# Performance work log

Hardware: AMD Instinct MI355X
Metric: run time of the kernel (lower is better)

## Reference

```python
import jax, jax.numpy as jnp
import numpy as np

N_NODES = 50000
N_EDGES = 800000

def _sage_conv(x, src, dst, W, b, n_nodes):
    # DGL SAGEConv aggregator_type='gcn':
    #   h_neigh = (sum_{u in N(v)} x_u + x_v) / (in_deg(v) + 1)
    #   out = h_neigh @ W.T + b   (fc_self unused for gcn aggregator)
    agg = jax.ops.segment_sum(x[src], dst, num_segments=n_nodes)  # [N, d]
    deg = jax.ops.segment_sum(jnp.ones((src.shape[0],), x.dtype), dst, num_segments=n_nodes)
    h = (agg + x) / (deg + 1.0)[:, None]
    return h @ W.T + b

def setup_inputs() -> dict:
    key = jax.random.key(0)
    ks = jax.random.split(key, 9)
    d_in, d_hid, d_out = 128, 128, 64
    x = jax.random.normal(ks[0], (N_NODES, d_in), dtype=jnp.float32)
    src = jax.random.randint(ks[1], (N_EDGES,), 0, N_NODES, dtype=jnp.int32)
    dst = jax.random.randint(ks[2], (N_EDGES,), 0, N_NODES, dtype=jnp.int32)
    def glorot(k, shape):
        fan = shape[0] + shape[1]
        return jax.random.normal(k, shape, dtype=jnp.float32) * jnp.sqrt(2.0 / fan)
    W1 = glorot(ks[3], (d_hid, d_in))
    b1 = jnp.zeros((d_hid,), jnp.float32)
    W2 = glorot(ks[4], (d_hid, d_hid))
    b2 = jnp.zeros((d_hid,), jnp.float32)
    W3 = glorot(ks[5], (d_out, d_hid))
    b3 = jnp.zeros((d_out,), jnp.float32)
    return {"x": x, "src": src, "dst": dst, "W1": W1, "b1": b1,
            "W2": W2, "b2": b2, "W3": W3, "b3": b3}

def reference(x, src, dst, W1, b1, W2, b2, W3, b3):
    n = x.shape[0]
    h = jax.nn.relu(_sage_conv(x, src, dst, W1, b1, n))
    h = jax.nn.relu(_sage_conv(h, src, dst, W2, b2, n))
    h = jax.nn.sigmoid(_sage_conv(h, src, dst, W3, b3, n))
    return h
```

## Files before the change

kernel.cpp:

```cpp
#include <hip/hip_runtime.h>
#include <hip/hip_bf16.h>
#include <math.h>


#define NFEAT 128
#define BSH   7
#define NBUKP 512
#define EPB2  1024
#define CAP   4000

typedef __attribute__((ext_vector_type(8))) short bf16x8;
typedef __attribute__((ext_vector_type(4))) float f32x4;

__device__ __forceinline__ unsigned short f2bf(float f) {
    unsigned u = __float_as_uint(f);
    u += 0x7fffu + ((u >> 16) & 1u);
    return (unsigned short)(u >> 16);
}
__device__ __forceinline__ float bflo(unsigned u) { return __uint_as_float(u << 16); }
__device__ __forceinline__ float bfhi(unsigned u) { return __uint_as_float(u & 0xffff0000u); }


__global__ __launch_bounds__(256) void build_scatter(const int* __restrict__ src,
                                                     const int* __restrict__ dst,
                                                     int* __restrict__ cursor,
                                                     unsigned long long* __restrict__ pairs,
                                                     int E) {
    __shared__ int hist[NBUKP];
    __shared__ int sc[NBUKP];
    __shared__ int lcur[NBUKP];
    __shared__ int lbase[NBUKP];
    __shared__ unsigned long long stage[EPB2];
    __shared__ int destIdx[EPB2];
    __shared__ int nLocalSh;

    const int t = threadIdx.x;
    hist[t] = 0; hist[t + 256] = 0;
    lcur[t] = 0; lcur[t + 256] = 0;
    __syncthreads();

    const int base = blockIdx.x * EPB2;
    int bb[EPB2 / 256];
    unsigned long long pr[EPB2 / 256];
#pragma unroll
    for (int j = 0; j < EPB2 / 256; ++j) {
        int e = base + t + 256 * j;
        bb[j] = -1;
        if (e < E) {
            int s = src[e], d = dst[e];
            int b = d >> BSH;
            bb[j] = b;
            pr[j] = ((unsigned long long)(unsigned)d << 32) | (unsigned)s;
            atomicAdd(&hist[b], 1);
        }
    }
    __syncthreads();
    sc[t] = hist[t]; sc[t + 256] = hist[t + 256];
    __syncthreads();
    for (int off = 1; off < NBUKP; off <<= 1) {
        int v0 = (t >= off) ? sc[t - off] : 0;
        int v1 = (t + 256 >= off) ? sc[t + 256 - off] : 0;
        __syncthreads();
        sc[t] += v0; sc[t + 256] += v1;
        __syncthreads();
    }
    if (t == 255) nLocalSh = sc[NBUKP - 1];
    sc[t] -= hist[t]; sc[t + 256] -= hist[t + 256];
    for (int b = t; b < NBUKP; b += 256) {
        int h = hist[b];
        if (h > 0) lbase[b] = atomicAdd(&cursor[b], h);
    }
    __syncthreads();
#pragma unroll
    for (int j = 0; j < EPB2 / 256; ++j) {
        int b = bb[j];
        if (b >= 0) {
            int slot = atomicAdd(&lcur[b], 1);
            int spos = sc[b] + slot;
            stage[spos] = pr[j];
            int rel = lbase[b] + slot;
            destIdx[spos] = (rel < CAP) ? (b * CAP + rel) : -1;
        }
    }
    __syncthreads();
    const int nLocal = nLocalSh;
#pragma unroll
    for (int j = 0; j < EPB2 / 256; ++j) {
        int i = t + 256 * j;
        if (i < nLocal && destIdx[i] >= 0) pairs[destIdx[i]] = stage[i];
    }
}


__global__ __launch_bounds__(256) void build_csr(const unsigned long long* __restrict__ pairs,
                                                 const int* __restrict__ cursor,
                                                 int* __restrict__ row_beg,
                                                 int* __restrict__ row_end,
                                                 float* __restrict__ deg_inv,
                                                 int* __restrict__ col_idx, int N) {
    __shared__ unsigned long long pairsL[CAP];
    __shared__ int srcS[CAP];
    __shared__ int nhist[128];
    __shared__ int npref[128];
    __shared__ int ncur[128];

    const int t = threadIdx.x;
    const int b = blockIdx.x;
    const int nodeBase = b << BSH;
    const int eBeg = b * CAP;
    int eCnt = cursor[b];
    if (eCnt > CAP) eCnt = CAP;

    if (t < 128) { nhist[t] = 0; ncur[t] = 0; }
    __syncthreads();

    for (int i = t; i < eCnt; i += 256) {
        unsigned long long p = pairs[eBeg + i];
        pairsL[i] = p;
        atomicAdd(&nhist[(int)(p >> 32) - nodeBase], 1);
    }
    __syncthreads();
    if (t < 128) npref[t] = nhist[t];
    __syncthreads();
    for (int off = 1; off < 128; off <<= 1) {
        int v = (t < 128 && t >= off) ? npref[t - off] : 0;
        __syncthreads();
        if (t < 128) npref[t] += v;
        __syncthreads();
    }
    if (t < 128) npref[t] -= nhist[t];
    if (t < 128 && nodeBase + t < N) {
        row_beg[nodeBase + t] = eBeg + npref[t];
        row_end[nodeBase + t] = eBeg + npref[t] + nhist[t];
        deg_inv[nodeBase + t] = 1.0f / (float)(nhist[t] + 1);
    }
    __syncthreads();
    for (int i = t; i < eCnt; i += 256) {
        unsigned long long p = pairsL[i];
        int d = (int)(p >> 32) - nodeBase;
        int slot = atomicAdd(&ncur[d], 1);
        srcS[npref[d] + slot] = (int)(unsigned)p;
    }
    __syncthreads();
    for (int i = t; i < eCnt; i += 256) col_idx[eBeg + i] = srcS[i];
}


__global__ __launch_bounds__(256) void cvt_all_kernel(const float* __restrict__ x,
                                                      const float* __restrict__ W1,
                                                      const float* __restrict__ W2,
                                                      const float* __restrict__ W3,
                                                      ushort* __restrict__ xb,
                                                      ushort* __restrict__ w1,
                                                      ushort* __restrict__ w2,
                                                      ushort* __restrict__ w3,
                                                      int nx, int n1, int n2, int n3) {
    int i = blockIdx.x * blockDim.x + threadIdx.x;
    const float* src; ushort* dst; int off;
    if (i < nx)                      { src = x;  dst = xb; off = i; }
    else if (i < nx + n1)            { src = W1; dst = w1; off = i - nx; }
    else if (i < nx + n1 + n2)       { src = W2; dst = w2; off = i - nx - n1; }
    else if (i < nx + n1 + n2 + n3)  { src = W3; dst = w3; off = i - nx - n1 - n2; }
    else return;
    float4 f = *(const float4*)(src + (size_t)off * 4);
    *(ushort4*)(dst + (size_t)off * 4) = make_ushort4(f2bf(f.x), f2bf(f.y), f2bf(f.z), f2bf(f.w));
}


#define ACC8(u)                                                     \
    a0 += bflo((u).x); a1 += bfhi((u).x);                           \
    a2 += bflo((u).y); a3 += bfhi((u).y);                           \
    a4 += bflo((u).z); a5 += bfhi((u).z);                           \
    a6 += bflo((u).w); a7 += bfhi((u).w);

template<int SECOND>
__global__ __launch_bounds__(256) void fused_agg_gemm_kernel(
        const ushort* __restrict__ Xb,
        const int* __restrict__ row_beg,
        const int* __restrict__ row_end,
        const float* __restrict__ deg_inv,
        const ushort* __restrict__ Wb,
        const float* __restrict__ bias,
        const ushort* __restrict__ W3b,
        const int* __restrict__ col_idx,
        ushort* __restrict__ outB, int N) {
    __shared__ ushort A[16][136];
    __shared__ ushort H2[SECOND ? 16 : 1][136];

    const int t    = threadIdx.x;
    const int w    = t >> 6;
    const int lane = t & 63;
    const int g    = lane >> 4;
    const int f    = lane & 15;
    const int base = blockIdx.x * 16;
    const uint4* X4 = (const uint4*)Xb;

#pragma unroll
    for (int i = 0; i < 4; ++i) {
        const int v = base + w * 4 + i;
        if (v < N) {
            const int beg = row_beg[v];
            const int end = row_end[v];

            float a0 = 0.f, a1 = 0.f, a2 = 0.f, a3 = 0.f;
            float a4 = 0.f, a5 = 0.f, a6 = 0.f, a7 = 0.f;
            int e = beg + g;
            for (; e + 12 < end; e += 16) {
                int s0 = col_idx[e];
                int s1 = col_idx[e + 4];
                int s2 = col_idx[e + 8];
                int s3 = col_idx[e + 12];
                uint4 u0 = X4[(size_t)s0 * 16 + f];
                uint4 u1 = X4[(size_t)s1 * 16 + f];
                uint4 u2 = X4[(size_t)s2 * 16 + f];
                uint4 u3 = X4[(size_t)s3 * 16 + f];
                ACC8(u0); ACC8(u1); ACC8(u2); ACC8(u3);
            }
            for (; e < end; e += 4) {
                uint4 u = X4[(size_t)col_idx[e] * 16 + f];
                ACC8(u);
            }
            a0 += __shfl_xor(a0, 16, 64); a0 += __shfl_xor(a0, 32, 64);
            a1 += __shfl_xor(a1, 16, 64); a1 += __shfl_xor(a1, 32, 64);
            a2 += __shfl_xor(a2, 16, 64); a2 += __shfl_xor(a2, 32, 64);
            a3 += __shfl_xor(a3, 16, 64); a3 += __shfl_xor(a3, 32, 64);
            a4 += __shfl_xor(a4, 16, 64); a4 += __shfl_xor(a4, 32, 64);
            a5 += __shfl_xor(a5, 16, 64); a5 += __shfl_xor(a5, 32, 64);
            a6 += __shfl_xor(a6, 16, 64); a6 += __shfl_xor(a6, 32, 64);
            a7 += __shfl_xor(a7, 16, 64); a7 += __shfl_xor(a7, 32, 64);
            if (g == 0) {
                uint4 us = X4[(size_t)v * 16 + f];
                float inv = deg_inv[v];
                uint4 r;
                r.x = (unsigned)f2bf((a0 + bflo(us.x)) * inv) | ((unsigned)f2bf((a1 + bfhi(us.x)) * inv) << 16);
                r.y = (unsigned)f2bf((a2 + bflo(us.y)) * inv) | ((unsigned)f2bf((a3 + bfhi(us.y)) * inv) << 16);
                r.z = (unsigned)f2bf((a4 + bflo(us.z)) * inv) | ((unsigned)f2bf((a5 + bfhi(us.z)) * inv) << 16);
                r.w = (unsigned)f2bf((a6 + bflo(us.w)) * inv) | ((unsigned)f2bf((a7 + bfhi(us.w)) * inv) << 16);
                ((uint4*)&A[w * 4 + i][0])[f] = r;
            }
        }
    }
    __syncthreads();

    const int m    = lane & 15;
    const int quad = lane >> 4;
    f32x4 acc0 = {0.f, 0.f, 0.f, 0.f};
    f32x4 acc1 = {0.f, 0.f, 0.f, 0.f};
    {
        const ushort* arow = &A[m][quad * 8];
        const ushort* wrow = Wb + (size_t)(w * 32 + m) * NFEAT + quad * 8;
#pragma unroll
        for (int k0 = 0; k0 < NFEAT; k0 += 32) {
            bf16x8 a  = *(const bf16x8*)(arow + k0);
            bf16x8 bA = *(const bf16x8*)(wrow + k0);
            bf16x8 bB = *(const bf16x8*)(wrow + 16 * NFEAT + k0);
            acc0 = __builtin_amdgcn_mfma_f32_16x16x32_bf16(a, bA, acc0, 0, 0, 0);
            acc1 = __builtin_amdgcn_mfma_f32_16x16x32_bf16(a, bB, acc1, 0, 0, 0);
        }
    }
    const float bv0 = bias[w * 32 + m];
    const float bv1 = bias[w * 32 + 16 + m];

    if (!SECOND) {
#pragma unroll
        for (int r = 0; r < 4; ++r) {
            int row = base + quad * 4 + r;
            if (row < N) {
                outB[(size_t)row * NFEAT + w * 32 + m]      = f2bf(fmaxf(acc0[r] + bv0, 0.f));
                outB[(size_t)row * NFEAT + w * 32 + 16 + m] = f2bf(fmaxf(acc1[r] + bv1, 0.f));
            }
        }
    } else {
#pragma unroll
        for (int r = 0; r < 4; ++r) {
            H2[quad * 4 + r][w * 32 + m]      = f2bf(fmaxf(acc0[r] + bv0, 0.f));
            H2[quad * 4 + r][w * 32 + 16 + m] = f2bf(fmaxf(acc1[r] + bv1, 0.f));
        }
        __syncthreads();
        f32x4 acc3 = {0.f, 0.f, 0.f, 0.f};
        const ushort* hrow  = &H2[m][quad * 8];
        const ushort* w3row = W3b + (size_t)(w * 16 + m) * NFEAT + quad * 8;
#pragma unroll
        for (int k0 = 0; k0 < NFEAT; k0 += 32) {
            bf16x8 a = *(const bf16x8*)(hrow + k0);
            bf16x8 b = *(const bf16x8*)(w3row + k0);
            acc3 = __builtin_amdgcn_mfma_f32_16x16x32_bf16(a, b, acc3, 0, 0, 0);
        }
#pragma unroll
        for (int r = 0; r < 4; ++r) {
            int row = base + quad * 4 + r;
            if (row < N) outB[(size_t)row * 64 + w * 16 + m] = f2bf(acc3[r]);
        }
    }
}


__global__ __launch_bounds__(256) void agg64_sigmoid_kernel(const ushort* __restrict__ Gb,
                                                            const int* __restrict__ row_beg,
                                                            const int* __restrict__ row_end,
                                                            const float* __restrict__ deg_inv,
                                                            const int* __restrict__ col_idx,
                                                            const float* __restrict__ bias,
                                                            float* __restrict__ out, int N) {
    const int wp   = blockIdx.x * (blockDim.x >> 6) + (threadIdx.x >> 6);
    const int lane = threadIdx.x & 63;
    const int half = lane >> 5;
    const int hl   = lane & 31;
    const int v    = wp * 2 + half;
    const bool act = (v < N);

    int beg = 0, end = 0;
    if (act) { beg = row_beg[v]; end = row_end[v]; }
    const int deg = end - beg;
    const unsigned* Gu = (const unsigned*)Gb;

    int cidx = 0;
    if (hl < deg) cidx = col_idx[beg + hl];

    float a0 = 0.f, a1 = 0.f, b0 = 0.f, b1 = 0.f;
    float c0 = 0.f, c1 = 0.f, d0 = 0.f, d1 = 0.f;
    const int nfast = deg < 32 ? deg : 32;
    int j = 0;
    for (; j + 3 < nfast; j += 4) {
        int s0 = __shfl(cidx, j + 0, 32);
        int s1 = __shfl(cidx, j + 1, 32);
        int s2 = __shfl(cidx, j + 2, 32);
        int s3 = __shfl(cidx, j + 3, 32);
        unsigned u0 = Gu[(size_t)s0 * 32 + hl];
        unsigned u1 = Gu[(size_t)s1 * 32 + hl];
        unsigned u2 = Gu[(size_t)s2 * 32 + hl];
        unsigned u3 = Gu[(size_t)s3 * 32 + hl];
        a0 += bflo(u0); a1 += bfhi(u0);
        b0 += bflo(u1); b1 += bfhi(u1);
        c0 += bflo(u2); c1 += bfhi(u2);
        d0 += bflo(u3); d1 += bfhi(u3);
    }
    for (; j < nfast; ++j) {
        int s0 = __shfl(cidx, j, 32);
        unsigned u0 = Gu[(size_t)s0 * 32 + hl];
        a0 += bflo(u0); a1 += bfhi(u0);
    }
    for (int e = beg + 32; e < end; ++e) {
        unsigned u0 = Gu[(size_t)col_idx[e] * 32 + hl];
        a0 += bflo(u0); a1 += bfhi(u0);
    }
    if (act) {
        unsigned us = Gu[(size_t)v * 32 + hl];
        float inv = deg_inv[v];
        float r0 = (a0 + b0 + c0 + d0 + bflo(us)) * inv + bias[hl * 2 + 0];
        float r1 = (a1 + b1 + c1 + d1 + bfhi(us)) * inv + bias[hl * 2 + 1];
        r0 = 1.0f / (1.0f + __expf(-r0));
        r1 = 1.0f / (1.0f + __expf(-r1));
        *(float2*)(out + (size_t)v * 64 + hl * 2) = make_float2(r0, r1);
    }
}


static inline size_t align256(size_t x) { return (x + 255) & ~(size_t)255; }

extern "C" void kernel_launch(void* const* d_in, const int* in_sizes, int n_in,
                              void* d_out, int out_size, void* d_ws, size_t ws_size,
                              hipStream_t stream) {
    const float* x   = (const float*)d_in[0];
    const int*   src = (const int*)d_in[1];
    const int*   dst = (const int*)d_in[2];
    const float* W1  = (const float*)d_in[3];
    const float* b1  = (const float*)d_in[4];
    const float* W2  = (const float*)d_in[5];
    const float* b2  = (const float*)d_in[6];
    const float* W3  = (const float*)d_in[7];
    const float* b3  = (const float*)d_in[8];
    float*       out = (float*)d_out;

    const int N = in_sizes[0] / NFEAT;
    const int E = in_sizes[1];
    const int D_OUT = in_sizes[7] / NFEAT;
    const int NBUK = (N + (1 << BSH) - 1) >> BSH;
    const int SBLK = (E + EPB2 - 1) / EPB2;

    char* ws = (char*)d_ws;
    int* row_beg      = (int*)ws;  ws += align256((size_t)N * 4);
    int* row_end      = (int*)ws;  ws += align256((size_t)N * 4);
    float* deg_inv    = (float*)ws; ws += align256((size_t)N * 4);
    int* cursor       = (int*)ws;  ws += align256((size_t)NBUK * 4);
    int* col_idx      = (int*)ws;  ws += align256((size_t)NBUK * CAP * 4);
    ushort* w1bf      = (ushort*)ws; ws += align256((size_t)NFEAT * NFEAT * 2);
    ushort* w2bf      = (ushort*)ws; ws += align256((size_t)NFEAT * NFEAT * 2);
    ushort* w3bf      = (ushort*)ws; ws += align256((size_t)D_OUT * NFEAT * 2);
    ushort* xbf       = (ushort*)ws; ws += align256((size_t)N * NFEAT * 2);
    ushort* h1bf      = (ushort*)ws; ws += align256((size_t)N * NFEAT * 2);
    ushort* gbf = xbf;
    unsigned long long* pairs = (unsigned long long*)h1bf;

    hipMemsetAsync(cursor, 0, (size_t)NBUK * 4, stream);
    build_scatter<<<SBLK, 256, 0, stream>>>(src, dst, cursor, pairs, E);
    build_csr<<<NBUK, 256, 0, stream>>>(pairs, cursor, row_beg, row_end, deg_inv, col_idx, N);

    const int nx = N * NFEAT / 4;
    const int n1 = NFEAT * NFEAT / 4, n2 = NFEAT * NFEAT / 4, n3 = D_OUT * NFEAT / 4;
    cvt_all_kernel<<<(nx + n1 + n2 + n3 + 255) / 256, 256, 0, stream>>>(
        x, W1, W2, W3, xbf, w1bf, w2bf, w3bf, nx, n1, n2, n3);

    const int fusedBlocks = (N + 15) / 16;
    const int agg64Blocks = (N + 7) / 8;

    fused_agg_gemm_kernel<0><<<fusedBlocks, 256, 0, stream>>>(
        xbf, row_beg, row_end, deg_inv, w1bf, b1, nullptr, col_idx, h1bf, N);
    fused_agg_gemm_kernel<1><<<fusedBlocks, 256, 0, stream>>>(
        h1bf, row_beg, row_end, deg_inv, w2bf, b2, w3bf, col_idx, gbf, N);
    agg64_sigmoid_kernel<<<agg64Blocks, 256, 0, stream>>>(
        gbf, row_beg, row_end, deg_inv, col_idx, b3, out, N);
}
```

Baseline: 237.8 us.

## Split final 64-wide features into two planes and fold cursor reset into convert kernel

The second fused GEMM kernel now writes its 64-column output as two 32-column planes, and the final aggregation kernel is rewritten to handle one plane per block. In that kernel each wavefront processes four nodes, with lane groups striding over edges and a shuffle reduction at the end. Splitting into planes shrinks each gather row to 64 bytes, which should improve cache locality for the random neighbour gathers. The cursor memset is removed and the cursor is instead zeroed inside the conversion kernel, which now runs before the CSR build; this saves one launch but serialises the graph build behind the conversion.

```diff
diff --git a/kernel.cpp b/kernel.cpp
--- a/kernel.cpp
+++ b/kernel.cpp
@@ -154,8 +154,10 @@
                                                       ushort* __restrict__ w1,
                                                       ushort* __restrict__ w2,
                                                       ushort* __restrict__ w3,
+                                                      int* __restrict__ cursor, int nbuk,
                                                       int nx, int n1, int n2, int n3) {
     int i = blockIdx.x * blockDim.x + threadIdx.x;
+    if (i < nbuk) cursor[i] = 0;
     const float* src; ushort* dst; int off;
     if (i < nx)                      { src = x;  dst = xb; off = i; }
     else if (i < nx + n1)            { src = W1; dst = w1; off = i - nx; }
@@ -289,69 +291,70 @@
 #pragma unroll
         for (int r = 0; r < 4; ++r) {
             int row = base + quad * 4 + r;
-            if (row < N) outB[(size_t)row * 64 + w * 16 + m] = f2bf(acc3[r]);
-        }
-    }
-}
-
-
-__global__ __launch_bounds__(256) void agg64_sigmoid_kernel(const ushort* __restrict__ Gb,
-                                                            const int* __restrict__ row_beg,
-                                                            const int* __restrict__ row_end,
-                                                            const float* __restrict__ deg_inv,
-                                                            const int* __restrict__ col_idx,
-                                                            const float* __restrict__ bias,
-                                                            float* __restrict__ out, int N) {
-    const int wp   = blockIdx.x * (blockDim.x >> 6) + (threadIdx.x >> 6);
+            if (row < N)
+                outB[((size_t)(w >> 1) * N + row) * 32 + (w & 1) * 16 + m] = f2bf(acc3[r]);
+        }
+    }
+}
+
+
+__global__ __launch_bounds__(256) void agg64_plane_kernel(
+        const ushort* __restrict__ Gpl,
+        const int* __restrict__ row_beg,
+        const int* __restrict__ row_end,
+        const float* __restrict__ deg_inv,
+        const int* __restrict__ col_idx,
+        const float* __restrict__ bias,
+        float* __restrict__ out, int N) {
+    const int s    = blockIdx.x & 1;
+    const int tile = blockIdx.x >> 1;
+    const int w    = threadIdx.x >> 6;
     const int lane = threadIdx.x & 63;
-    const int half = lane >> 5;
-    const int hl   = lane & 31;
-    const int v    = wp * 2 + half;
-    const bool act = (v < N);
-
-    int beg = 0, end = 0;
-    if (act) { beg = row_beg[v]; end = row_end[v]; }
-    const int deg = end - beg;
-    const unsigned* Gu = (const unsigned*)Gb;
-
-    int cidx = 0;
-    if (hl < deg) cidx = col_idx[beg + hl];
-
-    float a0 = 0.f, a1 = 0.f, b0 = 0.f, b1 = 0.f;
-    float c0 = 0.f, c1 = 0.f, d0 = 0.f, d1 = 0.f;
-    const int nfast = deg < 32 ? deg : 32;
-    int j = 0;
-    for (; j + 3 < nfast; j += 4) {
-        int s0 = __shfl(cidx, j + 0, 32);
-        int s1 = __shfl(cidx, j + 1, 32);
-        int s2 = __shfl(cidx, j + 2, 32);
-        int s3 = __shfl(cidx, j + 3, 32);
-        unsigned u0 = Gu[(size_t)s0 * 32 + hl];
-        unsigned u1 = Gu[(size_t)s1 * 32 + hl];
-        unsigned u2 = Gu[(size_t)s2 * 32 + hl];
-        unsigned u3 = Gu[(size_t)s3 * 32 + hl];
-        a0 += bflo(u0); a1 += bfhi(u0);
-        b0 += bflo(u1); b1 += bfhi(u1);
-        c0 += bflo(u2); c1 += bfhi(u2);
-        d0 += bflo(u3); d1 += bfhi(u3);
-    }
-    for (; j < nfast; ++j) {
-        int s0 = __shfl(cidx, j, 32);
-        unsigned u0 = Gu[(size_t)s0 * 32 + hl];
-        a0 += bflo(u0); a1 += bfhi(u0);
-    }
-    for (int e = beg + 32; e < end; ++e) {
-        unsigned u0 = Gu[(size_t)col_idx[e] * 32 + hl];
-        a0 += bflo(u0); a1 += bfhi(u0);
-    }
-    if (act) {
-        unsigned us = Gu[(size_t)v * 32 + hl];
-        float inv = deg_inv[v];
-        float r0 = (a0 + b0 + c0 + d0 + bflo(us)) * inv + bias[hl * 2 + 0];
-        float r1 = (a1 + b1 + c1 + d1 + bfhi(us)) * inv + bias[hl * 2 + 1];
-        r0 = 1.0f / (1.0f + __expf(-r0));
-        r1 = 1.0f / (1.0f + __expf(-r1));
-        *(float2*)(out + (size_t)v * 64 + hl * 2) = make_float2(r0, r1);
+    const int g    = lane >> 4;
+    const int f    = lane & 15;
+    const unsigned* P = (const unsigned*)Gpl + (size_t)s * N * 16;
+
+#pragma unroll
+    for (int i = 0; i < 4; ++i) {
+        const int v = tile * 16 + w * 4 + i;
+        if (v >= N) continue;
+        const int beg = row_beg[v];
+        const int end = row_end[v];
+
+        float a0 = 0.f, a1 = 0.f, b0 = 0.f, b1 = 0.f;
+        float c0 = 0.f, c1 = 0.f, d0 = 0.f, d1 = 0.f;
+        int e = beg + g;
+        for (; e + 12 < end; e += 16) {
+            int s0 = col_idx[e];
+            int s1 = col_idx[e + 4];
+            int s2 = col_idx[e + 8];
+            int s3 = col_idx[e + 12];
+            unsigned u0 = P[(size_t)s0 * 16 + f];
+            unsigned u1 = P[(size_t)s1 * 16 + f];
+            unsigned u2 = P[(size_t)s2 * 16 + f];
+            unsigned u3 = P[(size_t)s3 * 16 + f];
+            a0 += bflo(u0); a1 += bfhi(u0);
+            b0 += bflo(u1); b1 += bfhi(u1);
+            c0 += bflo(u2); c1 += bfhi(u2);
+            d0 += bflo(u3); d1 += bfhi(u3);
+        }
+        for (; e < end; e += 4) {
+            unsigned u0 = P[(size_t)col_idx[e] * 16 + f];
+            a0 += bflo(u0); a1 += bfhi(u0);
+        }
+        a0 += b0 + c0 + d0;
+        a1 += b1 + c1 + d1;
+        a0 += __shfl_xor(a0, 16, 64); a0 += __shfl_xor(a0, 32, 64);
+        a1 += __shfl_xor(a1, 16, 64); a1 += __shfl_xor(a1, 32, 64);
+        if (g == 0) {
+            unsigned us = P[(size_t)v * 16 + f];
+            float inv = deg_inv[v];
+            float r0 = (a0 + bflo(us)) * inv + bias[s * 32 + 2 * f + 0];
+            float r1 = (a1 + bfhi(us)) * inv + bias[s * 32 + 2 * f + 1];
+            r0 = 1.0f / (1.0f + __expf(-r0));
+            r1 = 1.0f / (1.0f + __expf(-r1));
+            *(float2*)(out + (size_t)v * 64 + s * 32 + 2 * f) = make_float2(r0, r1);
+        }
     }
 }
 
@@ -389,25 +392,24 @@
     ushort* w3bf      = (ushort*)ws; ws += align256((size_t)D_OUT * NFEAT * 2);
     ushort* xbf       = (ushort*)ws; ws += align256((size_t)N * NFEAT * 2);
     ushort* h1bf      = (ushort*)ws; ws += align256((size_t)N * NFEAT * 2);
-    ushort* gbf = xbf;
+    ushort* gpl = xbf;
     unsigned long long* pairs = (unsigned long long*)h1bf;
-
-    hipMemsetAsync(cursor, 0, (size_t)NBUK * 4, stream);
-    build_scatter<<<SBLK, 256, 0, stream>>>(src, dst, cursor, pairs, E);
-    build_csr<<<NBUK, 256, 0, stream>>>(pairs, cursor, row_beg, row_end, deg_inv, col_idx, N);
 
     const int nx = N * NFEAT / 4;
     const int n1 = NFEAT * NFEAT / 4, n2 = NFEAT * NFEAT / 4, n3 = D_OUT * NFEAT / 4;
     cvt_all_kernel<<<(nx + n1 + n2 + n3 + 255) / 256, 256, 0, stream>>>(
-        x, W1, W2, W3, xbf, w1bf, w2bf, w3bf, nx, n1, n2, n3);
+        x, W1, W2, W3, xbf, w1bf, w2bf, w3bf, cursor, NBUK, nx, n1, n2, n3);
+
+    build_scatter<<<SBLK, 256, 0, stream>>>(src, dst, cursor, pairs, E);
+    build_csr<<<NBUK, 256, 0, stream>>>(pairs, cursor, row_beg, row_end, deg_inv, col_idx, N);
 
     const int fusedBlocks = (N + 15) / 16;
-    const int agg64Blocks = (N + 7) / 8;
+    const int tiles       = (N + 15) / 16;
 
     fused_agg_gemm_kernel<0><<<fusedBlocks, 256, 0, stream>>>(
         xbf, row_beg, row_end, deg_inv, w1bf, b1, nullptr, col_idx, h1bf, N);
     fused_agg_gemm_kernel<1><<<fusedBlocks, 256, 0, stream>>>(
-        h1bf, row_beg, row_end, deg_inv, w2bf, b2, w3bf, col_idx, gbf, N);
-    agg64_sigmoid_kernel<<<agg64Blocks, 256, 0, stream>>>(
-        gbf, row_beg, row_end, deg_inv, col_idx, b3, out, N);
-}
+        h1bf, row_beg, row_end, deg_inv, w2bf, b2, w3bf, col_idx, gpl, N);
+    agg64_plane_kernel<<<tiles * 2, 256, 0, stream>>>(
+        gpl, row_beg, row_end, deg_inv, col_idx, b3, out, N);
+}
```

After: 256.1 us. 1.08x slower.
